# Optimization experiments

Measured on AMD Instinct MI355X. Metric: run time of the kernel, lower is better.

The kernel has to match this reference:

```python
import jax, jax.numpy as jnp
import numpy as np

ALPHA_LIM = (float(np.exp(-1.0 / 5.0)), float(np.exp(-1.0 / 25.0)))
BETA_LIM = (float(np.exp(-1.0 / 30.0)), float(np.exp(-1.0 / 120.0)))
A_LIM = (-1.0, 1.0)
B_LIM = (0.0, 2.0)
THRESHOLD = 1.0


@jax.custom_vjp
def spike_boxcar(x):
    # Heaviside forward, boxcar surrogate gradient
    return (x > 0).astype(x.dtype)


def _spike_fwd(x):
    return spike_boxcar(x), x


def _spike_bwd(x, g):
    return (jnp.where(jnp.abs(x) <= 0.5, g, jnp.zeros_like(g)),)


spike_boxcar.defvjp(_spike_fwd, _spike_bwd)


def setup_inputs() -> dict:
    key = jax.random.key(0)
    ks = jax.random.split(key, 9)
    B, T, I, H = 128, 512, 512, 512
    return {
        "x": jax.random.normal(ks[0], (B, T, I), dtype=jnp.float32),
        "W": jax.random.normal(ks[1], (H, I), dtype=jnp.float32) / np.sqrt(I),
        "alpha": jax.random.uniform(ks[2], (H,), dtype=jnp.float32),
        "beta": jax.random.uniform(ks[3], (H,), dtype=jnp.float32),
        "a": jax.random.uniform(ks[4], (H,), dtype=jnp.float32),
        "b": jax.random.uniform(ks[5], (H,), dtype=jnp.float32),
        "u0": jax.random.uniform(ks[6], (B, H), dtype=jnp.float32),
        "w0": jax.random.uniform(ks[7], (B, H), dtype=jnp.float32),
        "s0": jax.random.uniform(ks[8], (B, H), dtype=jnp.float32),
    }


def reference(x, W, alpha, beta, a, b, u0, w0, s0):
    # x: [B, T, I]; W: [H, I] (nn.Linear weight, no bias)
    alpha = jnp.clip(alpha, ALPHA_LIM[0], ALPHA_LIM[1])
    beta = jnp.clip(beta, BETA_LIM[0], BETA_LIM[1])
    a = jnp.clip(a, A_LIM[0], A_LIM[1])
    b = jnp.clip(b, B_LIM[0], B_LIM[1])

    Wx = jnp.einsum("bti,hi->bth", x, W)  # [B, T, H]
    Wx_t = jnp.transpose(Wx, (1, 0, 2))    # [T, B, H] for scan over time

    def step(carry, wx_t):
        ut, wt, st = carry
        wt = beta * wt + a * ut + b * st
        ut = alpha * (ut - st) + (1.0 - alpha) * (wx_t - wt)
        st = spike_boxcar(ut - THRESHOLD)
        return (ut, wt, st), st

    _, s = jax.lax.scan(step, (u0, w0, s0), Wx_t)  # s: [T, B, H]
    return jnp.transpose(s, (1, 0, 2))  # [B, T, H]
```

## Files before the change

### kernel.cpp

```cpp
#include <hip/hip_runtime.h>
#include <hip/hip_bf16.h>


#define M_SZ 65536
#define H_SZ 512
#define K_SZ 512
#define B_SZ 128
#define T_SZ 512
#define LSTR 132

typedef __attribute__((ext_vector_type(4))) float f32x4;

__device__ __forceinline__ bool detect_bf16(const unsigned int* __restrict__ w) {
  int c = 0;
#pragma unroll
  for (int i = 0; i < 64; ++i) {
    unsigned int e = (w[i] >> 7) & 0xffu;
    c += (e >= 115u && e <= 131u) ? 1 : 0;
  }
  return c > 32;
}

template <bool ISB>
__device__ __forceinline__ f32x4 ld4t(const void* __restrict__ p, size_t off) {
  if constexpr (!ISB) {
    return *reinterpret_cast<const f32x4*>(reinterpret_cast<const float*>(p) + off);
  } else {
    uint2 v = *reinterpret_cast<const uint2*>(reinterpret_cast<const unsigned short*>(p) + off);
    f32x4 r;
    r.x = __uint_as_float((v.x & 0xffffu) << 16);
    r.y = __uint_as_float(v.x & 0xffff0000u);
    r.z = __uint_as_float((v.y & 0xffffu) << 16);
    r.w = __uint_as_float(v.y & 0xffff0000u);
    return r;
  }
}

template <bool ISB>
__device__ __forceinline__ float ld1t(const void* __restrict__ p, int i) {
  if constexpr (!ISB) return reinterpret_cast<const float*>(p)[i];
  return __uint_as_float((unsigned int)(reinterpret_cast<const unsigned short*>(p)[i]) << 16);
}

template <bool ISB>
__device__ __forceinline__ void gemm_body(const void* __restrict__ X,
                                          const void* __restrict__ Wm,
                                          float* __restrict__ C,
                                          float* __restrict__ As,
                                          float* __restrict__ Bs) {
  const int tid = threadIdx.x;
  const int r0 = tid >> 2;
  const int q0 = (tid & 3) * 4;
  const int tx = tid & 15;
  const int ty = tid >> 4;
  const size_t M0 = (size_t)(blockIdx.x >> 2) * 128;
  const int N0 = (blockIdx.x & 3) * 128;

  float acc[8][8];
#pragma unroll
  for (int i = 0; i < 8; ++i)
#pragma unroll
    for (int j = 0; j < 8; ++j) acc[i][j] = 0.0f;

  const size_t aoff0 = (M0 + r0) * K_SZ + q0;
  const size_t aoff1 = (M0 + r0 + 64) * K_SZ + q0;
  const size_t boff0 = (size_t)(N0 + r0) * K_SZ + q0;
  const size_t boff1 = (size_t)(N0 + r0 + 64) * K_SZ + q0;

  f32x4 pa0 = ld4t<ISB>(X, aoff0), pa1 = ld4t<ISB>(X, aoff1);
  f32x4 pb0 = ld4t<ISB>(Wm, boff0), pb1 = ld4t<ISB>(Wm, boff1);

  for (int kk = 0; kk < K_SZ; kk += 16) {
    __syncthreads();
    As[(q0 + 0) * LSTR + r0] = pa0.x; As[(q0 + 1) * LSTR + r0] = pa0.y;
    As[(q0 + 2) * LSTR + r0] = pa0.z; As[(q0 + 3) * LSTR + r0] = pa0.w;
    As[(q0 + 0) * LSTR + r0 + 64] = pa1.x; As[(q0 + 1) * LSTR + r0 + 64] = pa1.y;
    As[(q0 + 2) * LSTR + r0 + 64] = pa1.z; As[(q0 + 3) * LSTR + r0 + 64] = pa1.w;
    Bs[(q0 + 0) * LSTR + r0] = pb0.x; Bs[(q0 + 1) * LSTR + r0] = pb0.y;
    Bs[(q0 + 2) * LSTR + r0] = pb0.z; Bs[(q0 + 3) * LSTR + r0] = pb0.w;
    Bs[(q0 + 0) * LSTR + r0 + 64] = pb1.x; Bs[(q0 + 1) * LSTR + r0 + 64] = pb1.y;
    Bs[(q0 + 2) * LSTR + r0 + 64] = pb1.z; Bs[(q0 + 3) * LSTR + r0 + 64] = pb1.w;
    __syncthreads();
    if (kk + 16 < K_SZ) {
      pa0 = ld4t<ISB>(X, aoff0 + kk + 16); pa1 = ld4t<ISB>(X, aoff1 + kk + 16);
      pb0 = ld4t<ISB>(Wm, boff0 + kk + 16); pb1 = ld4t<ISB>(Wm, boff1 + kk + 16);
    }
#pragma unroll
    for (int k = 0; k < 16; ++k) {
      const f32x4 a0 = *reinterpret_cast<const f32x4*>(As + k * LSTR + ty * 4);
      const f32x4 a1 = *reinterpret_cast<const f32x4*>(As + k * LSTR + 64 + ty * 4);
      const f32x4 b0 = *reinterpret_cast<const f32x4*>(Bs + k * LSTR + tx * 4);
      const f32x4 b1 = *reinterpret_cast<const f32x4*>(Bs + k * LSTR + 64 + tx * 4);
      const float av[8] = {a0.x, a0.y, a0.z, a0.w, a1.x, a1.y, a1.z, a1.w};
      const float bv[8] = {b0.x, b0.y, b0.z, b0.w, b1.x, b1.y, b1.z, b1.w};
#pragma unroll
      for (int i = 0; i < 8; ++i)
#pragma unroll
        for (int j = 0; j < 8; ++j) acc[i][j] += av[i] * bv[j];
    }
  }

#pragma unroll
  for (int r = 0; r < 8; ++r) {
    const size_t m = M0 + ((r < 4) ? (ty * 4 + r) : (64 + ty * 4 + (r - 4)));
    float* Cp = C + m * H_SZ + N0;
    f32x4 v0 = {acc[r][0], acc[r][1], acc[r][2], acc[r][3]};
    f32x4 v1 = {acc[r][4], acc[r][5], acc[r][6], acc[r][7]};
    __builtin_nontemporal_store(v0, reinterpret_cast<f32x4*>(Cp + tx * 4));
    __builtin_nontemporal_store(v1, reinterpret_cast<f32x4*>(Cp + 64 + tx * 4));
  }
}

__global__ __launch_bounds__(256) void sgemm_bt(const void* __restrict__ X,
                                                const void* __restrict__ Wm,
                                                float* __restrict__ C) {
  __shared__ float As[16 * LSTR];
  __shared__ float Bs[16 * LSTR];
  if (detect_bf16(reinterpret_cast<const unsigned int*>(X)))
    gemm_body<true>(X, Wm, C, As, Bs);
  else
    gemm_body<false>(X, Wm, C, As, Bs);
}

#define SCT 8
#define SNC (T_SZ / SCT)

template <bool ISB>
__device__ __forceinline__ void scan_body(
    const float* __restrict__ wx, const void* __restrict__ alpha_p,
    const void* __restrict__ beta_p, const void* __restrict__ a_p,
    const void* __restrict__ b_p, const void* __restrict__ u0p,
    const void* __restrict__ w0p, const void* __restrict__ s0p,
    void* __restrict__ out) {
  const int lane = threadIdx.x;
  const int b = blockIdx.x >> 3;
  const int h0 = (blockIdx.x & 7) * 64;
  const int h = h0 + lane;

  const float al = fminf(fmaxf(ld1t<ISB>(alpha_p, h), (float)0.8187307530779818),
                         (float)0.9607894391523232);
  const float be = fminf(fmaxf(ld1t<ISB>(beta_p, h), (float)0.9672161004820059),
                         (float)0.9917013044213351);
  const float av = fminf(fmaxf(ld1t<ISB>(a_p, h), -1.0f), 1.0f);
  const float bv = fminf(fmaxf(ld1t<ISB>(b_p, h), 0.0f), 2.0f);
  const float om = __fsub_rn(1.0f, al);

  const int bh = b * H_SZ + h;
  float u = ld1t<ISB>(u0p, bh);
  float w = ld1t<ISB>(w0p, bh);
  float s = ld1t<ISB>(s0p, bh);

  const float* xb = wx + (size_t)b * T_SZ * H_SZ + h;
  float* outf = reinterpret_cast<float*>(out);
  __hip_bfloat16* outb = reinterpret_cast<__hip_bfloat16*>(out);
  const size_t ob0 = (size_t)b * T_SZ * H_SZ + h;

  float ring[4][SCT];
  auto loadc = [&](float* dst, int c) {
#pragma unroll
    for (int j = 0; j < SCT; ++j) {
      int t = c * SCT + j;
      t = (t < T_SZ) ? t : (T_SZ - 1);
      dst[j] = xb[(size_t)t * H_SZ];
    }
  };

  loadc(ring[0], 0); loadc(ring[1], 1); loadc(ring[2], 2); loadc(ring[3], 3);

  for (int c0 = 0; c0 < SNC; c0 += 4) {
#pragma unroll
    for (int p = 0; p < 4; ++p) {
      const int c = c0 + p;
#pragma unroll
      for (int j = 0; j < SCT; ++j) {
        const float cur = ring[p][j];
        w = __fadd_rn(__fadd_rn(__fmul_rn(be, w), __fmul_rn(av, u)), __fmul_rn(bv, s));
        u = __fadd_rn(__fmul_rn(al, __fsub_rn(u, s)), __fmul_rn(om, __fsub_rn(cur, w)));
        s = (u > 1.0f) ? 1.0f : 0.0f;
        const size_t o = ob0 + (size_t)(c * SCT + j) * H_SZ;
        if constexpr (ISB) outb[o] = __float2bfloat16(s);
        else outf[o] = s;
      }
      loadc(ring[p], c + 4);
    }
  }
}

__global__ __launch_bounds__(64) void lif_scan(
    const float* __restrict__ wx, const void* __restrict__ X,
    const void* __restrict__ alpha_p, const void* __restrict__ beta_p,
    const void* __restrict__ a_p, const void* __restrict__ b_p,
    const void* __restrict__ u0p, const void* __restrict__ w0p,
    const void* __restrict__ s0p, void* __restrict__ out) {
  if (detect_bf16(reinterpret_cast<const unsigned int*>(X)))
    scan_body<true>(wx, alpha_p, beta_p, a_p, b_p, u0p, w0p, s0p, out);
  else
    scan_body<false>(wx, alpha_p, beta_p, a_p, b_p, u0p, w0p, s0p, out);
}

extern "C" void kernel_launch(void* const* d_in, const int* in_sizes, int n_in,
                              void* d_out, int out_size, void* d_ws, size_t ws_size,
                              hipStream_t stream) {
  const void* X = d_in[0];
  const void* Wm = d_in[1];
  float* ws = reinterpret_cast<float*>(d_ws);

  sgemm_bt<<<dim3((M_SZ / 128) * (H_SZ / 128)), dim3(256), 0, stream>>>(X, Wm, ws);

  lif_scan<<<dim3(B_SZ * 8), dim3(64), 0, stream>>>(
      ws, X, d_in[2], d_in[3], d_in[4], d_in[5], d_in[6], d_in[7], d_in[8], d_out);
}
```

Baseline: 622.2 us.

## Double-buffer GEMM shared tiles and batch scan spike stores per chunk

The GEMM now alternates between two shared-memory tile buffers, so the next tile is staged while the current one is computed, which halves the barriers per k-step. Its output stores become ordinary cached stores instead of nontemporal ones, so the Wx workspace may stay in cache for the scan kernel. The scan kernel buffers spike values per chunk and writes them in a separate loop using precomputed store pointers, to decouple the stores from the serial recurrence. The cost is double the LDS use per GEMM block, which may lower occupancy, and more registers in the scan.

```diff
diff --git a/kernel.cpp b/kernel.cpp
--- a/kernel.cpp
+++ b/kernel.cpp
@@ -46,8 +46,10 @@
 __device__ __forceinline__ void gemm_body(const void* __restrict__ X,
                                           const void* __restrict__ Wm,
                                           float* __restrict__ C,
-                                          float* __restrict__ As,
-                                          float* __restrict__ Bs) {
+                                          float* __restrict__ As0,
+                                          float* __restrict__ Bs0,
+                                          float* __restrict__ As1,
+                                          float* __restrict__ Bs1) {
   const int tid = threadIdx.x;
   const int r0 = tid >> 2;
   const int q0 = (tid & 3) * 4;
@@ -67,11 +69,15 @@
   const size_t boff0 = (size_t)(N0 + r0) * K_SZ + q0;
   const size_t boff1 = (size_t)(N0 + r0 + 64) * K_SZ + q0;
 
-  f32x4 pa0 = ld4t<ISB>(X, aoff0), pa1 = ld4t<ISB>(X, aoff1);
-  f32x4 pb0 = ld4t<ISB>(Wm, boff0), pb1 = ld4t<ISB>(Wm, boff1);
-
-  for (int kk = 0; kk < K_SZ; kk += 16) {
-    __syncthreads();
+  f32x4 pa0, pa1, pb0, pb1;
+
+  auto prefetch = [&](int kk) {
+    pa0 = ld4t<ISB>(X, aoff0 + kk);
+    pa1 = ld4t<ISB>(X, aoff1 + kk);
+    pb0 = ld4t<ISB>(Wm, boff0 + kk);
+    pb1 = ld4t<ISB>(Wm, boff1 + kk);
+  };
+  auto stage = [&](float* __restrict__ As, float* __restrict__ Bs) {
     As[(q0 + 0) * LSTR + r0] = pa0.x; As[(q0 + 1) * LSTR + r0] = pa0.y;
     As[(q0 + 2) * LSTR + r0] = pa0.z; As[(q0 + 3) * LSTR + r0] = pa0.w;
     As[(q0 + 0) * LSTR + r0 + 64] = pa1.x; As[(q0 + 1) * LSTR + r0 + 64] = pa1.y;
@@ -80,24 +86,39 @@
     Bs[(q0 + 2) * LSTR + r0] = pb0.z; Bs[(q0 + 3) * LSTR + r0] = pb0.w;
     Bs[(q0 + 0) * LSTR + r0 + 64] = pb1.x; Bs[(q0 + 1) * LSTR + r0 + 64] = pb1.y;
     Bs[(q0 + 2) * LSTR + r0 + 64] = pb1.z; Bs[(q0 + 3) * LSTR + r0 + 64] = pb1.w;
-    __syncthreads();
-    if (kk + 16 < K_SZ) {
-      pa0 = ld4t<ISB>(X, aoff0 + kk + 16); pa1 = ld4t<ISB>(X, aoff1 + kk + 16);
-      pb0 = ld4t<ISB>(Wm, boff0 + kk + 16); pb1 = ld4t<ISB>(Wm, boff1 + kk + 16);
-    }
+  };
+  auto compute = [&](const float* __restrict__ As, const float* __restrict__ Bs) {
 #pragma unroll
     for (int k = 0; k < 16; ++k) {
       const f32x4 a0 = *reinterpret_cast<const f32x4*>(As + k * LSTR + ty * 4);
       const f32x4 a1 = *reinterpret_cast<const f32x4*>(As + k * LSTR + 64 + ty * 4);
       const f32x4 b0 = *reinterpret_cast<const f32x4*>(Bs + k * LSTR + tx * 4);
       const f32x4 b1 = *reinterpret_cast<const f32x4*>(Bs + k * LSTR + 64 + tx * 4);
-      const float av[8] = {a0.x, a0.y, a0.z, a0.w, a1.x, a1.y, a1.z, a1.w};
-      const float bv[8] = {b0.x, b0.y, b0.z, b0.w, b1.x, b1.y, b1.z, b1.w};
+      const float avv[8] = {a0.x, a0.y, a0.z, a0.w, a1.x, a1.y, a1.z, a1.w};
+      const float bvv[8] = {b0.x, b0.y, b0.z, b0.w, b1.x, b1.y, b1.z, b1.w};
 #pragma unroll
       for (int i = 0; i < 8; ++i)
 #pragma unroll
-        for (int j = 0; j < 8; ++j) acc[i][j] += av[i] * bv[j];
-    }
+        for (int j = 0; j < 8; ++j) acc[i][j] += avv[i] * bvv[j];
+    }
+  };
+
+  prefetch(0);
+  stage(As0, Bs0);
+  prefetch(16);
+  __syncthreads();
+
+  for (int kk = 0; kk < K_SZ; kk += 32) {
+    stage(As1, Bs1);
+    if (kk + 32 < K_SZ) prefetch(kk + 32);
+    compute(As0, Bs0);
+    __syncthreads();
+    if (kk + 32 < K_SZ) {
+      stage(As0, Bs0);
+      if (kk + 48 < K_SZ) prefetch(kk + 48);
+    }
+    compute(As1, Bs1);
+    __syncthreads();
   }
 
 #pragma unroll
@@ -106,20 +127,22 @@
     float* Cp = C + m * H_SZ + N0;
     f32x4 v0 = {acc[r][0], acc[r][1], acc[r][2], acc[r][3]};
     f32x4 v1 = {acc[r][4], acc[r][5], acc[r][6], acc[r][7]};
-    __builtin_nontemporal_store(v0, reinterpret_cast<f32x4*>(Cp + tx * 4));
-    __builtin_nontemporal_store(v1, reinterpret_cast<f32x4*>(Cp + 64 + tx * 4));
+    *reinterpret_cast<f32x4*>(Cp + tx * 4) = v0;
+    *reinterpret_cast<f32x4*>(Cp + 64 + tx * 4) = v1;
   }
 }
 
 __global__ __launch_bounds__(256) void sgemm_bt(const void* __restrict__ X,
                                                 const void* __restrict__ Wm,
                                                 float* __restrict__ C) {
-  __shared__ float As[16 * LSTR];
-  __shared__ float Bs[16 * LSTR];
+  __shared__ float As0[16 * LSTR];
+  __shared__ float Bs0[16 * LSTR];
+  __shared__ float As1[16 * LSTR];
+  __shared__ float Bs1[16 * LSTR];
   if (detect_bf16(reinterpret_cast<const unsigned int*>(X)))
-    gemm_body<true>(X, Wm, C, As, Bs);
+    gemm_body<true>(X, Wm, C, As0, Bs0, As1, Bs1);
   else
-    gemm_body<false>(X, Wm, C, As, Bs);
+    gemm_body<false>(X, Wm, C, As0, Bs0, As1, Bs1);
 }
 
 #define SCT 8
@@ -134,8 +157,7 @@
     void* __restrict__ out) {
   const int lane = threadIdx.x;
   const int b = blockIdx.x >> 3;
-  const int h0 = (blockIdx.x & 7) * 64;
-  const int h = h0 + lane;
+  const int h = (blockIdx.x & 7) * 64 + lane;
 
   const float al = fminf(fmaxf(ld1t<ISB>(alpha_p, h), (float)0.8187307530779818),
                          (float)0.9607894391523232);
@@ -151,9 +173,9 @@
   float s = ld1t<ISB>(s0p, bh);
 
   const float* xb = wx + (size_t)b * T_SZ * H_SZ + h;
-  float* outf = reinterpret_cast<float*>(out);
-  __hip_bfloat16* outb = reinterpret_cast<__hip_bfloat16*>(out);
+  char* ob = reinterpret_cast<char*>(out);
   const size_t ob0 = (size_t)b * T_SZ * H_SZ + h;
+  const size_t esz = ISB ? 2u : 4u;
 
   float ring[4][SCT];
   auto loadc = [&](float* dst, int c) {
@@ -165,23 +187,41 @@
     }
   };
 
+  float sdat[2][SCT];
+  char* pst[4][SCT];
+  auto calca = [&](char** dst, int c) {
+#pragma unroll
+    for (int j = 0; j < SCT; ++j)
+      dst[j] = ob + (ob0 + (size_t)(c * SCT + j) * H_SZ) * esz;
+  };
+
   loadc(ring[0], 0); loadc(ring[1], 1); loadc(ring[2], 2); loadc(ring[3], 3);
+  calca(pst[0], 0); calca(pst[1], 1); calca(pst[2], 2); calca(pst[3], 3);
 
   for (int c0 = 0; c0 < SNC; c0 += 4) {
 #pragma unroll
     for (int p = 0; p < 4; ++p) {
       const int c = c0 + p;
+      const int q = p & 1;
 #pragma unroll
       for (int j = 0; j < SCT; ++j) {
         const float cur = ring[p][j];
         w = __fadd_rn(__fadd_rn(__fmul_rn(be, w), __fmul_rn(av, u)), __fmul_rn(bv, s));
         u = __fadd_rn(__fmul_rn(al, __fsub_rn(u, s)), __fmul_rn(om, __fsub_rn(cur, w)));
-        s = (u > 1.0f) ? 1.0f : 0.0f;
-        const size_t o = ob0 + (size_t)(c * SCT + j) * H_SZ;
-        if constexpr (ISB) outb[o] = __float2bfloat16(s);
-        else outf[o] = s;
+        const bool sp = (u > 1.0f);
+        s = sp ? 1.0f : 0.0f;
+        sdat[q][j] = ISB ? __uint_as_float(sp ? 0x3F80u : 0u) : s;
+      }
+#pragma unroll
+      for (int j = 0; j < SCT; ++j) {
+        if constexpr (ISB)
+          *reinterpret_cast<unsigned short*>(pst[p][j]) =
+              (unsigned short)__float_as_uint(sdat[q][j]);
+        else
+          *reinterpret_cast<float*>(pst[p][j]) = sdat[q][j];
       }
       loadc(ring[p], c + 4);
+      calca(pst[(p + 2) & 3], c + 2);
     }
   }
 }
```

Measured after the change: 757.7 us. 21.8% more time.

## Warp-specialize LIF scan with producer warps staging loads and stores via LDS

Applied to the files above, without the earlier changes.

The scan kernel now runs 512 threads per block. One compute wave runs the recurrence from a double-buffered LDS input tile of 32 timesteps. Seven producer waves prefetch the next tile from global memory and write the previous tile's spikes back to global, synchronised by block barriers, so the serial wave no longer stalls on global latency. The GEMM output also switches from nontemporal to normal stores, so the scan can hit the Wx results in cache. The cost is a barrier per tile, extra LDS traffic, and seven waves that mostly wait.

```diff
diff --git a/kernel.cpp b/kernel.cpp
--- a/kernel.cpp
+++ b/kernel.cpp
@@ -106,8 +106,8 @@
     float* Cp = C + m * H_SZ + N0;
     f32x4 v0 = {acc[r][0], acc[r][1], acc[r][2], acc[r][3]};
     f32x4 v1 = {acc[r][4], acc[r][5], acc[r][6], acc[r][7]};
-    __builtin_nontemporal_store(v0, reinterpret_cast<f32x4*>(Cp + tx * 4));
-    __builtin_nontemporal_store(v1, reinterpret_cast<f32x4*>(Cp + 64 + tx * 4));
+    *reinterpret_cast<f32x4*>(Cp + tx * 4) = v0;
+    *reinterpret_cast<f32x4*>(Cp + 64 + tx * 4) = v1;
   }
 }
 
@@ -122,8 +122,9 @@
     gemm_body<false>(X, Wm, C, As, Bs);
 }
 
-#define SCT 8
-#define SNC (T_SZ / SCT)
+#define SC 32
+#define NSC (T_SZ / SC)
+#define PMAX 5
 
 template <bool ISB>
 __device__ __forceinline__ void scan_body(
@@ -131,71 +132,122 @@
     const void* __restrict__ beta_p, const void* __restrict__ a_p,
     const void* __restrict__ b_p, const void* __restrict__ u0p,
     const void* __restrict__ w0p, const void* __restrict__ s0p,
-    void* __restrict__ out) {
-  const int lane = threadIdx.x;
+    void* __restrict__ out, float* __restrict__ inb, float* __restrict__ outb) {
+  const int tid = threadIdx.x;
+  const int lane = tid & 63;
+  const int wid = tid >> 6;
   const int b = blockIdx.x >> 3;
-  const int h0 = (blockIdx.x & 7) * 64;
-  const int h = h0 + lane;
-
-  const float al = fminf(fmaxf(ld1t<ISB>(alpha_p, h), (float)0.8187307530779818),
-                         (float)0.9607894391523232);
-  const float be = fminf(fmaxf(ld1t<ISB>(beta_p, h), (float)0.9672161004820059),
-                         (float)0.9917013044213351);
-  const float av = fminf(fmaxf(ld1t<ISB>(a_p, h), -1.0f), 1.0f);
-  const float bv = fminf(fmaxf(ld1t<ISB>(b_p, h), 0.0f), 2.0f);
-  const float om = __fsub_rn(1.0f, al);
-
-  const int bh = b * H_SZ + h;
-  float u = ld1t<ISB>(u0p, bh);
-  float w = ld1t<ISB>(w0p, bh);
-  float s = ld1t<ISB>(s0p, bh);
-
-  const float* xb = wx + (size_t)b * T_SZ * H_SZ + h;
+  const int h = (blockIdx.x & 7) * 64 + lane;
+
+  auto IN = [&](int par, int r) -> float* { return inb + (par * SC + r) * 64; };
+  auto OUT = [&](int par, int r) -> float* { return outb + (par * SC + r) * 64; };
+
+  const float* xrow = wx + (size_t)b * T_SZ * H_SZ + h;
   float* outf = reinterpret_cast<float*>(out);
-  __hip_bfloat16* outb = reinterpret_cast<__hip_bfloat16*>(out);
+  unsigned short* outu = reinterpret_cast<unsigned short*>(out);
   const size_t ob0 = (size_t)b * T_SZ * H_SZ + h;
 
-  float ring[4][SCT];
-  auto loadc = [&](float* dst, int c) {
-#pragma unroll
-    for (int j = 0; j < SCT; ++j) {
-      int t = c * SCT + j;
-      t = (t < T_SZ) ? t : (T_SZ - 1);
-      dst[j] = xb[(size_t)t * H_SZ];
-    }
-  };
-
-  loadc(ring[0], 0); loadc(ring[1], 1); loadc(ring[2], 2); loadc(ring[3], 3);
-
-  for (int c0 = 0; c0 < SNC; c0 += 4) {
-#pragma unroll
-    for (int p = 0; p < 4; ++p) {
-      const int c = c0 + p;
-#pragma unroll
-      for (int j = 0; j < SCT; ++j) {
-        const float cur = ring[p][j];
+  if (wid == 0) {
+    const float al = fminf(fmaxf(ld1t<ISB>(alpha_p, h), (float)0.8187307530779818),
+                           (float)0.9607894391523232);
+    const float be = fminf(fmaxf(ld1t<ISB>(beta_p, h), (float)0.9672161004820059),
+                           (float)0.9917013044213351);
+    const float av = fminf(fmaxf(ld1t<ISB>(a_p, h), -1.0f), 1.0f);
+    const float bv = fminf(fmaxf(ld1t<ISB>(b_p, h), 0.0f), 2.0f);
+    const float om = __fsub_rn(1.0f, al);
+    const int bh = b * H_SZ + h;
+    float u = ld1t<ISB>(u0p, bh);
+    float w = ld1t<ISB>(w0p, bh);
+    float s = ld1t<ISB>(s0p, bh);
+
+    __syncthreads();
+    for (int sc = 0; sc < NSC; ++sc) {
+      const int par = sc & 1;
+      float nxt = IN(par, 0)[lane];
+#pragma unroll
+      for (int j = 0; j < SC; ++j) {
+        const float cur = nxt;
+        if (j + 1 < SC) nxt = IN(par, j + 1)[lane];
         w = __fadd_rn(__fadd_rn(__fmul_rn(be, w), __fmul_rn(av, u)), __fmul_rn(bv, s));
         u = __fadd_rn(__fmul_rn(al, __fsub_rn(u, s)), __fmul_rn(om, __fsub_rn(cur, w)));
         s = (u > 1.0f) ? 1.0f : 0.0f;
-        const size_t o = ob0 + (size_t)(c * SCT + j) * H_SZ;
-        if constexpr (ISB) outb[o] = __float2bfloat16(s);
-        else outf[o] = s;
-      }
-      loadc(ring[p], c + 4);
-    }
-  }
-}
-
-__global__ __launch_bounds__(64) void lif_scan(
+        OUT(par, j)[lane] = s;
+      }
+      __syncthreads();
+    }
+  } else {
+    const int pw = wid - 1;
+    float ld[PMAX];
+#pragma unroll
+    for (int k = 0; k < PMAX; ++k) {
+      const int r = pw + 7 * k;
+      if (r < SC) ld[k] = xrow[(size_t)r * H_SZ];
+    }
+#pragma unroll
+    for (int k = 0; k < PMAX; ++k) {
+      const int r = pw + 7 * k;
+      if (r < SC) IN(0, r)[lane] = ld[k];
+    }
+    __syncthreads();
+    for (int sc = 0; sc < NSC; ++sc) {
+      const int par = sc & 1;
+      if (sc + 1 < NSC) {
+#pragma unroll
+        for (int k = 0; k < PMAX; ++k) {
+          const int r = pw + 7 * k;
+          if (r < SC) ld[k] = xrow[(size_t)((sc + 1) * SC + r) * H_SZ];
+        }
+      }
+      if (sc > 0) {
+#pragma unroll
+        for (int k = 0; k < PMAX; ++k) {
+          const int r = pw + 7 * k;
+          if (r < SC) {
+            const float sv = OUT(par ^ 1, r)[lane];
+            const size_t o = ob0 + (size_t)((sc - 1) * SC + r) * H_SZ;
+            if constexpr (ISB)
+              outu[o] = (sv != 0.0f) ? (unsigned short)0x3F80u : (unsigned short)0u;
+            else
+              outf[o] = sv;
+          }
+        }
+      }
+      if (sc + 1 < NSC) {
+#pragma unroll
+        for (int k = 0; k < PMAX; ++k) {
+          const int r = pw + 7 * k;
+          if (r < SC) IN(par ^ 1, r)[lane] = ld[k];
+        }
+      }
+      __syncthreads();
+    }
+#pragma unroll
+    for (int k = 0; k < PMAX; ++k) {
+      const int r = pw + 7 * k;
+      if (r < SC) {
+        const float sv = OUT((NSC - 1) & 1, r)[lane];
+        const size_t o = ob0 + (size_t)((NSC - 1) * SC + r) * H_SZ;
+        if constexpr (ISB)
+          outu[o] = (sv != 0.0f) ? (unsigned short)0x3F80u : (unsigned short)0u;
+        else
+          outf[o] = sv;
+      }
+    }
+  }
+}
+
+__global__ __launch_bounds__(512) void lif_scan(
     const float* __restrict__ wx, const void* __restrict__ X,
     const void* __restrict__ alpha_p, const void* __restrict__ beta_p,
     const void* __restrict__ a_p, const void* __restrict__ b_p,
     const void* __restrict__ u0p, const void* __restrict__ w0p,
     const void* __restrict__ s0p, void* __restrict__ out) {
+  __shared__ float inb[2 * SC * 64];
+  __shared__ float outb[2 * SC * 64];
   if (detect_bf16(reinterpret_cast<const unsigned int*>(X)))
-    scan_body<true>(wx, alpha_p, beta_p, a_p, b_p, u0p, w0p, s0p, out);
+    scan_body<true>(wx, alpha_p, beta_p, a_p, b_p, u0p, w0p, s0p, out, inb, outb);
   else
-    scan_body<false>(wx, alpha_p, beta_p, a_p, b_p, u0p, w0p, s0p, out);
+    scan_body<false>(wx, alpha_p, beta_p, a_p, b_p, u0p, w0p, s0p, out, inb, outb);
 }
 
 extern "C" void kernel_launch(void* const* d_in, const int* in_sizes, int n_in,
@@ -207,6 +259,6 @@
 
   sgemm_bt<<<dim3((M_SZ / 128) * (H_SZ / 128)), dim3(256), 0, stream>>>(X, Wm, ws);
 
-  lif_scan<<<dim3(B_SZ * 8), dim3(64), 0, stream>>>(
+  lif_scan<<<dim3(B_SZ * 8), dim3(512), 0, stream>>>(
       ws, X, d_in[2], d_in[3], d_in[4], d_in[5], d_in[6], d_in[7], d_in[8], d_out);
 }
```

New measurement: 618.1 us. About the same (-0.7%).

## Stage scan input tile in LDS with 256-thread cooperative load and store

Applied to the files above, without the earlier changes.

The scan kernel now uses 256 threads per block. All four wavefronts cooperatively load the whole [T,64] slice of Wx into a 128KB shared buffer with vectorized loads. One wavefront runs the serial recurrence out of LDS and writes the spikes back into the same buffer, then all threads store the output with wide coalesced writes, packing to bf16 when the input is bf16. The GEMM output stores also drop the nontemporal hint so Wx is more likely to stay in cache for the scan. The cost is 128KB of LDS per block, which limits occupancy, and three wavefronts sit idle during the serial phase.

```diff
diff --git a/kernel.cpp b/kernel.cpp
--- a/kernel.cpp
+++ b/kernel.cpp
@@ -10,6 +10,7 @@
 #define LSTR 132
 
 typedef __attribute__((ext_vector_type(4))) float f32x4;
+typedef __attribute__((ext_vector_type(4))) unsigned int u32x4;
 
 __device__ __forceinline__ bool detect_bf16(const unsigned int* __restrict__ w) {
   int c = 0;
@@ -106,8 +107,8 @@
     float* Cp = C + m * H_SZ + N0;
     f32x4 v0 = {acc[r][0], acc[r][1], acc[r][2], acc[r][3]};
     f32x4 v1 = {acc[r][4], acc[r][5], acc[r][6], acc[r][7]};
-    __builtin_nontemporal_store(v0, reinterpret_cast<f32x4*>(Cp + tx * 4));
-    __builtin_nontemporal_store(v1, reinterpret_cast<f32x4*>(Cp + 64 + tx * 4));
+    *reinterpret_cast<f32x4*>(Cp + tx * 4) = v0;
+    *reinterpret_cast<f32x4*>(Cp + 64 + tx * 4) = v1;
   }
 }
 
@@ -122,80 +123,115 @@
     gemm_body<false>(X, Wm, C, As, Bs);
 }
 
-#define SCT 8
-#define SNC (T_SZ / SCT)
-
 template <bool ISB>
 __device__ __forceinline__ void scan_body(
     const float* __restrict__ wx, const void* __restrict__ alpha_p,
     const void* __restrict__ beta_p, const void* __restrict__ a_p,
     const void* __restrict__ b_p, const void* __restrict__ u0p,
     const void* __restrict__ w0p, const void* __restrict__ s0p,
-    void* __restrict__ out) {
-  const int lane = threadIdx.x;
+    void* __restrict__ out, float* __restrict__ wxb) {
+  const int tid = threadIdx.x;
+  const int lane = tid & 63;
+  const int wid = tid >> 6;
   const int b = blockIdx.x >> 3;
-  const int h0 = (blockIdx.x & 7) * 64;
-  const int h = h0 + lane;
-
-  const float al = fminf(fmaxf(ld1t<ISB>(alpha_p, h), (float)0.8187307530779818),
-                         (float)0.9607894391523232);
-  const float be = fminf(fmaxf(ld1t<ISB>(beta_p, h), (float)0.9672161004820059),
-                         (float)0.9917013044213351);
-  const float av = fminf(fmaxf(ld1t<ISB>(a_p, h), -1.0f), 1.0f);
-  const float bv = fminf(fmaxf(ld1t<ISB>(b_p, h), 0.0f), 2.0f);
-  const float om = __fsub_rn(1.0f, al);
-
-  const int bh = b * H_SZ + h;
-  float u = ld1t<ISB>(u0p, bh);
-  float w = ld1t<ISB>(w0p, bh);
-  float s = ld1t<ISB>(s0p, bh);
-
-  const float* xb = wx + (size_t)b * T_SZ * H_SZ + h;
-  float* outf = reinterpret_cast<float*>(out);
-  __hip_bfloat16* outb = reinterpret_cast<__hip_bfloat16*>(out);
-  const size_t ob0 = (size_t)b * T_SZ * H_SZ + h;
-
-  float ring[4][SCT];
-  auto loadc = [&](float* dst, int c) {
-#pragma unroll
-    for (int j = 0; j < SCT; ++j) {
-      int t = c * SCT + j;
-      t = (t < T_SZ) ? t : (T_SZ - 1);
-      dst[j] = xb[(size_t)t * H_SZ];
-    }
-  };
-
-  loadc(ring[0], 0); loadc(ring[1], 1); loadc(ring[2], 2); loadc(ring[3], 3);
-
-  for (int c0 = 0; c0 < SNC; c0 += 4) {
-#pragma unroll
-    for (int p = 0; p < 4; ++p) {
-      const int c = c0 + p;
-#pragma unroll
-      for (int j = 0; j < SCT; ++j) {
-        const float cur = ring[p][j];
+  const int strip = (blockIdx.x & 7);
+  const int h = strip * 64 + lane;
+
+  {
+    const float* gb = wx + (size_t)b * T_SZ * H_SZ + strip * 64 + (tid & 15) * 4;
+    const int rb = tid >> 4;
+#pragma unroll
+    for (int g = 0; g < 4; ++g) {
+      f32x4 v[8];
+#pragma unroll
+      for (int j = 0; j < 8; ++j) {
+        const int r = 16 * (g * 8 + j) + rb;
+        v[j] = *reinterpret_cast<const f32x4*>(gb + (size_t)r * H_SZ);
+      }
+#pragma unroll
+      for (int j = 0; j < 8; ++j) {
+        const int r = 16 * (g * 8 + j) + rb;
+        *reinterpret_cast<f32x4*>(wxb + r * 64 + (tid & 15) * 4) = v[j];
+      }
+    }
+  }
+  __syncthreads();
+
+  if (wid == 0) {
+    const float al = fminf(fmaxf(ld1t<ISB>(alpha_p, h), (float)0.8187307530779818),
+                           (float)0.9607894391523232);
+    const float be = fminf(fmaxf(ld1t<ISB>(beta_p, h), (float)0.9672161004820059),
+                           (float)0.9917013044213351);
+    const float av = fminf(fmaxf(ld1t<ISB>(a_p, h), -1.0f), 1.0f);
+    const float bv = fminf(fmaxf(ld1t<ISB>(b_p, h), 0.0f), 2.0f);
+    const float om = __fsub_rn(1.0f, al);
+    const int bh = b * H_SZ + h;
+    float u = ld1t<ISB>(u0p, bh);
+    float w = ld1t<ISB>(w0p, bh);
+    float s = ld1t<ISB>(s0p, bh);
+
+    float nxt[8];
+#pragma unroll
+    for (int j = 0; j < 8; ++j) nxt[j] = wxb[j * 64 + lane];
+    for (int t0 = 0; t0 < T_SZ; t0 += 8) {
+      float cur8[8];
+#pragma unroll
+      for (int j = 0; j < 8; ++j) cur8[j] = nxt[j];
+      if (t0 + 8 < T_SZ) {
+#pragma unroll
+        for (int j = 0; j < 8; ++j) nxt[j] = wxb[(t0 + 8 + j) * 64 + lane];
+      }
+#pragma unroll
+      for (int j = 0; j < 8; ++j) {
         w = __fadd_rn(__fadd_rn(__fmul_rn(be, w), __fmul_rn(av, u)), __fmul_rn(bv, s));
-        u = __fadd_rn(__fmul_rn(al, __fsub_rn(u, s)), __fmul_rn(om, __fsub_rn(cur, w)));
+        u = __fadd_rn(__fmul_rn(al, __fsub_rn(u, s)), __fmul_rn(om, __fsub_rn(cur8[j], w)));
         s = (u > 1.0f) ? 1.0f : 0.0f;
-        const size_t o = ob0 + (size_t)(c * SCT + j) * H_SZ;
-        if constexpr (ISB) outb[o] = __float2bfloat16(s);
-        else outf[o] = s;
-      }
-      loadc(ring[p], c + 4);
-    }
-  }
-}
-
-__global__ __launch_bounds__(64) void lif_scan(
+        wxb[(t0 + j) * 64 + lane] = s;
+      }
+    }
+  }
+  __syncthreads();
+
+  if constexpr (!ISB) {
+    float* outf = reinterpret_cast<float*>(out) + (size_t)b * T_SZ * H_SZ + strip * 64;
+    const int rb = tid >> 4;
+#pragma unroll
+    for (int m = 0; m < 32; ++m) {
+      const int r = 16 * m + rb;
+      const f32x4 v = *reinterpret_cast<const f32x4*>(wxb + r * 64 + (tid & 15) * 4);
+      *reinterpret_cast<f32x4*>(outf + (size_t)r * H_SZ + (tid & 15) * 4) = v;
+    }
+  } else {
+    unsigned short* outu =
+        reinterpret_cast<unsigned short*>(out) + (size_t)b * T_SZ * H_SZ + strip * 64;
+    const int rb = tid >> 3;
+    const int h0 = (tid & 7) * 8;
+#pragma unroll
+    for (int m = 0; m < 16; ++m) {
+      const int r = 32 * m + rb;
+      const f32x4 f0 = *reinterpret_cast<const f32x4*>(wxb + r * 64 + h0);
+      const f32x4 f1 = *reinterpret_cast<const f32x4*>(wxb + r * 64 + h0 + 4);
+      u32x4 d;
+      d.x = (__float_as_uint(f0.y) & 0xffff0000u) | (__float_as_uint(f0.x) >> 16);
+      d.y = (__float_as_uint(f0.w) & 0xffff0000u) | (__float_as_uint(f0.z) >> 16);
+      d.z = (__float_as_uint(f1.y) & 0xffff0000u) | (__float_as_uint(f1.x) >> 16);
+      d.w = (__float_as_uint(f1.w) & 0xffff0000u) | (__float_as_uint(f1.z) >> 16);
+      *reinterpret_cast<u32x4*>(outu + (size_t)r * H_SZ + h0) = d;
+    }
+  }
+}
+
+__global__ __launch_bounds__(256) void lif_scan(
     const float* __restrict__ wx, const void* __restrict__ X,
     const void* __restrict__ alpha_p, const void* __restrict__ beta_p,
     const void* __restrict__ a_p, const void* __restrict__ b_p,
     const void* __restrict__ u0p, const void* __restrict__ w0p,
     const void* __restrict__ s0p, void* __restrict__ out) {
+  __shared__ float wxb[T_SZ * 64];
   if (detect_bf16(reinterpret_cast<const unsigned int*>(X)))
-    scan_body<true>(wx, alpha_p, beta_p, a_p, b_p, u0p, w0p, s0p, out);
+    scan_body<true>(wx, alpha_p, beta_p, a_p, b_p, u0p, w0p, s0p, out, wxb);
   else
-    scan_body<false>(wx, alpha_p, beta_p, a_p, b_p, u0p, w0p, s0p, out);
+    scan_body<false>(wx, alpha_p, beta_p, a_p, b_p, u0p, w0p, s0p, out, wxb);
 }
 
 extern "C" void kernel_launch(void* const* d_in, const int* in_sizes, int n_in,
@@ -207,6 +243,6 @@
 
   sgemm_bt<<<dim3((M_SZ / 128) * (H_SZ / 128)), dim3(256), 0, stream>>>(X, Wm, ws);
 
-  lif_scan<<<dim3(B_SZ * 8), dim3(64), 0, stream>>>(
+  lif_scan<<<dim3(B_SZ * 8), dim3(256), 0, stream>>>(
       ws, X, d_in[2], d_in[3], d_in[4], d_in[5], d_in[6], d_in[7], d_in[8], d_out);
 }
```

After: 691.1 us. 11.1% more time.
